# Performance work log

Measured on AMD Instinct MI355X. Metric: run time of the kernel, lower is better.

Reference implementation:

```python
import jax, jax.numpy as jnp
import numpy as np

NUM_CLASSES = 2
THRESHOLD = 0.35
NEGPOS_RATIO = 3
VAR0, VAR1 = 0.1, 0.2
ALPHA = 1.0
B, P, G = 16, 131072, 64


def _iou(a, b):
    # a: [G,4] point-form gts, b: [P,4] point-form priors -> [G,P]
    tl = jnp.maximum(a[:, None, :2], b[None, :, :2])
    br = jnp.minimum(a[:, None, 2:], b[None, :, 2:])
    wh = jnp.clip(br - tl, 0.0)
    inter = wh[..., 0] * wh[..., 1]
    area_a = (a[:, 2] - a[:, 0]) * (a[:, 3] - a[:, 1])
    area_b = (b[:, 2] - b[:, 0]) * (b[:, 3] - b[:, 1])
    return inter / (area_a[:, None] + area_b[None, :] - inter)


def setup_inputs() -> dict:
    key = jax.random.key(0)
    k1, k2, k3, k4, k5, k6 = jax.random.split(key, 6)
    loc_preds = jax.random.normal(k1, (B, P, 4), jnp.float32)
    cls_preds = jax.random.normal(k2, (B, P, NUM_CLASSES), jnp.float32)
    # priors in center form [cx, cy, w, h]
    pcxy = jax.random.uniform(k3, (P, 2), jnp.float32)
    pwh = 0.02 + 0.15 * jax.random.uniform(k4, (P, 2), jnp.float32)
    priorbox = jnp.concatenate([pcxy, pwh], axis=1)
    # ground-truth boxes; stored as [y1,x1,y2,x2,label] so that the module's
    # column permutation [1,0,3,2] yields valid point-form [x1,y1,x2,y2]
    xy1 = 0.8 * jax.random.uniform(k5, (B, G, 2), jnp.float32)
    wh = 0.02 + 0.1 * jax.random.uniform(k6, (B, G, 2), jnp.float32)
    xy2 = xy1 + wh
    boxes_perm = jnp.stack([xy1[..., 1], xy1[..., 0], xy2[..., 1], xy2[..., 0]], axis=-1)
    labels = jnp.ones((B, G, 1), jnp.float32)  # single foreground class (face)
    targets = jnp.concatenate([boxes_perm, labels], axis=-1)
    return {"loc_preds": loc_preds, "cls_preds": cls_preds,
            "priorbox": priorbox, "targets": targets}


def _loss(loc_preds, cls_preds, priorbox, targets):
    priors_c = priorbox[: loc_preds.shape[1], :]
    priors_pt = jnp.concatenate(
        [priors_c[:, :2] - priors_c[:, 2:] / 2,
         priors_c[:, :2] + priors_c[:, 2:] / 2], axis=1)
    num_g = targets.shape[1]

    def match_one(t):
        gts = t[:, :4][:, jnp.array([1, 0, 3, 2])]  # -> point form [x1,y1,x2,y2]
        labels = t[:, 4]
        ov = _iou(gts, priors_pt)                    # [G,P]
        best_prior_idx = jnp.argmax(ov, axis=1)      # [G]
        bto = jnp.max(ov, axis=0)                    # [P] best gt overlap per prior
        bti = jnp.argmax(ov, axis=0)                 # [P]
        bto = bto.at[best_prior_idx].set(2.0)        # force best prior per gt
        bti = bti.at[best_prior_idx].set(jnp.arange(num_g))
        conf = jnp.where(bto < THRESHOLD, 0.0, labels[bti])
        m = gts[bti]                                 # [P,4] matched gt boxes
        g_cxcy = ((m[:, :2] + m[:, 2:]) / 2 - priors_c[:, :2]) / (VAR0 * priors_c[:, 2:])
        g_wh = jnp.log((m[:, 2:] - m[:, :2]) / priors_c[:, 2:]) / VAR1
        return conf, jnp.concatenate([g_cxcy, g_wh], axis=1)

    cls_batch, loc_batch = jax.vmap(match_one)(targets)
    cls_batch = jax.lax.stop_gradient(cls_batch)   # targets require no grad
    loc_batch = jax.lax.stop_gradient(loc_batch)

    pos = cls_batch > 0                              # [B,P]
    npos = jnp.sum(pos)

    # smooth-L1 over positive priors, mean over selected elements (size_average)
    d = loc_preds - loc_batch
    ad = jnp.abs(d)
    sl1 = jnp.where(ad < 1.0, 0.5 * d * d, ad - 0.5)
    loss_loc = jnp.sum(sl1 * pos[..., None]) / jnp.maximum(npos * 4, 1).astype(sl1.dtype)

    # per-prior CE loss for hard-negative mining
    ignore = cls_batch < 0
    lbl = jnp.where(ignore, 0.0, cls_batch).astype(jnp.int32)
    lse = jax.nn.logsumexp(cls_preds, axis=-1)       # [B,P]
    gathered = jnp.take_along_axis(cls_preds, lbl[..., None], axis=-1)[..., 0]
    loss_c = jnp.where(pos | ignore, 0.0, lse - gathered)
    # two-stage sort: rank of each prior by descending loss
    loss_idx = jnp.argsort(-loss_c, axis=1)
    idx_rank = jnp.argsort(loss_idx, axis=1)
    num_pos_img = jnp.sum(pos, axis=1, keepdims=True)
    num_neg = jnp.minimum(NEGPOS_RATIO * num_pos_img, pos.shape[1] - 1)
    neg = idx_rank < num_neg
    mask = pos | neg
    # cross-entropy over mined samples, mean over selected (size_average)
    loss_cls = jnp.sum((lse - gathered) * mask) / jnp.maximum(jnp.sum(mask), 1).astype(lse.dtype)

    loss = (loss_cls + ALPHA * loss_loc) / npos.astype(lse.dtype)
    return loss, loss_loc, loss_cls


def reference(loc_preds, cls_preds, priorbox, targets):
    return _loss(loc_preds, cls_preds, priorbox, targets)
```

## Files before the change

### kernel.cpp

```cpp
#include <hip/hip_runtime.h>

#define BB 16
#define PP 131072
#define GG 64
#define THRESH 0.35f
#define RMAX 0.086f
#define NCELL 32
#define NCHM 64
#define CPM 2048
#define NCHL 64
#define CPL 2048
#define NCC 64
#define CPC 2048

#define OFF_BESTP   0
#define OFF_BEST64  524288
#define OFF_H1TOT   532480
#define OFF_NPOSP   794624
#define OFF_PCP     798720
#define OFF_LOCP    802816
#define OFF_CIDX    806912
#define OFF_NEGS    806976
#define OFF_RESN    807040
#define OFF_RESK    807104
#define OFF_RESC    807168
#define OFF_RESL    807232
#define OFF_PU8     807296
#define OFF_KEYS    2904448
#define OFF_CAND    11293056

__global__ __launch_bounds__(256) void k_match(
    const float* __restrict__ priorbox, const float* __restrict__ targets,
    unsigned long long* __restrict__ bestp, unsigned char* __restrict__ pu8,
    unsigned* __restrict__ h1tot, unsigned* __restrict__ cidx,
    float* __restrict__ negs)
{
    __shared__ unsigned msk[2 * NCELL * NCELL];
    __shared__ float4 gxy[GG];
    __shared__ unsigned long long sbest[GG];
    const int b = blockIdx.y, chunk = blockIdx.x, tid = threadIdx.x;

    if (tid < 64) h1tot[b * 4096 + chunk * 64 + tid] = 0u;
    if (chunk == 0 && tid == 0) { cidx[b] = 0u; negs[b] = 0.f; }
    for (int i = tid; i < 2 * NCELL * NCELL; i += 256) msk[i] = 0u;
    if (tid < GG) {
        const float* t = targets + (size_t)(b * GG + tid) * 5;
        gxy[tid] = make_float4(t[1], t[0], t[3], t[2]);
        sbest[tid] = 0ull;
    }
    __syncthreads();

    {
        const int g = tid & 63, strip = tid >> 6;
        float4 a = gxy[g];
        int cx0 = max(0, (int)((a.x - RMAX) * (float)NCELL));
        int cx1 = min(NCELL - 1, (int)ceilf((a.z + RMAX) * (float)NCELL) - 1);
        int cy0 = max(0, (int)((a.y - RMAX) * (float)NCELL));
        int cy1 = min(NCELL - 1, (int)ceilf((a.w + RMAX) * (float)NCELL) - 1);
        unsigned bit = 1u << (g & 31);
        const int word = (g >> 5);
        for (int cy = cy0 + strip; cy <= cy1; cy += 4)
            for (int cx = cx0; cx <= cx1; cx++)
                atomicOr(&msk[2 * (cy * NCELL + cx) + word], bit);
    }
    __syncthreads();

#pragma unroll
    for (int j = 0; j < 8; j++) {
        const int p = chunk * CPM + j * 256 + tid;
        float4 pr = *reinterpret_cast<const float4*>(priorbox + (size_t)p * 4);
        float hx = 0.5f * pr.z, hy = 0.5f * pr.w;
        float px1 = pr.x - hx, py1 = pr.y - hy;
        float px2 = pr.x + hx, py2 = pr.y + hy;
        float par = (px2 - px1) * (py2 - py1);
        int cx = min(NCELL - 1, max(0, (int)(pr.x * (float)NCELL)));
        int cy = min(NCELL - 1, max(0, (int)(pr.y * (float)NCELL)));
        uint2 mm = *reinterpret_cast<uint2*>(&msk[2 * (cy * NCELL + cx)]);
        unsigned long long m = ((unsigned long long)mm.y << 32) | mm.x;
        const unsigned long long notp = (unsigned long long)(~(unsigned)p);
        float bv = -1.f; int bg = 0;
        while (m) {
            const int g0 = __ffsll(m) - 1; m &= m - 1;
            const bool has1 = (m != 0ull);
            const int g1 = has1 ? (__ffsll(m) - 1) : g0;
            if (has1) m &= m - 1;
            float4 a0 = gxy[g0];
            float4 a1 = gxy[g1];
            float w0 = fmaxf(fminf(a0.z, px2) - fmaxf(a0.x, px1), 0.f);
            float h0 = fmaxf(fminf(a0.w, py2) - fmaxf(a0.y, py1), 0.f);
            float w1 = fmaxf(fminf(a1.z, px2) - fmaxf(a1.x, px1), 0.f);
            float h1 = fmaxf(fminf(a1.w, py2) - fmaxf(a1.y, py1), 0.f);
            float ar0 = (a0.z - a0.x) * (a0.w - a0.y);
            float ar1 = (a1.z - a1.x) * (a1.w - a1.y);
            float i0 = w0 * h0, i1 = w1 * h1;
            float v0 = i0 * __builtin_amdgcn_rcpf(ar0 + par - i0);
            float v1 = i1 * __builtin_amdgcn_rcpf(ar1 + par - i1);
            if (v0 > bv) { bv = v0; bg = g0; }
            if (has1 && v1 > bv) { bv = v1; bg = g1; }
            if (v0 > 0.f)
                atomicMax(&sbest[g0],
                          (((unsigned long long)__float_as_uint(v0)) << 32) | notp);
            if (has1 && v1 > 0.f)
                atomicMax(&sbest[g1],
                          (((unsigned long long)__float_as_uint(v1)) << 32) | notp);
        }
        pu8[(size_t)b * PP + p] = (unsigned char)(bg | ((bv >= THRESH) ? 0x80 : 0));
    }

    __syncthreads();
    if (tid < GG) bestp[(b * NCHM + chunk) * GG + tid] = sbest[tid];
}

__global__ void k_bred(const unsigned long long* __restrict__ bestp,
                       unsigned long long* __restrict__ best64)
{
    const int b = blockIdx.x, g = threadIdx.x;
    unsigned long long m = 0ull;
#pragma unroll 8
    for (int c = 0; c < NCHM; c++) {
        unsigned long long v = bestp[(b * NCHM + c) * GG + g];
        m = v > m ? v : m;
    }
    best64[b * GG + g] = m;
}

__global__ __launch_bounds__(256) void k_loss(
    const float* __restrict__ loc_preds, const float* __restrict__ cls_preds,
    const float* __restrict__ priorbox, const float* __restrict__ targets,
    const unsigned long long* __restrict__ best64, const unsigned char* __restrict__ pu8,
    unsigned* __restrict__ keys, unsigned* __restrict__ h1tot,
    int* __restrict__ nposp, float* __restrict__ pcp, float* __restrict__ locp)
{
    __shared__ unsigned hcnt[4096];
    __shared__ unsigned ovr[CPL];
    __shared__ float4 gxy[GG];
    __shared__ float glab[GG];
    __shared__ float sred[8];
    __shared__ int sredi[4];
    const int b = blockIdx.y, chunk = blockIdx.x, tid = threadIdx.x;
    const int lane = tid & 63, wid = tid >> 6;

    for (int i = tid; i < 4096; i += 256) hcnt[i] = 0u;
    for (int i = tid; i < CPL; i += 256) ovr[i] = 0u;
    if (tid < GG) {
        const float* t = targets + (size_t)(b * GG + tid) * 5;
        gxy[tid] = make_float4(t[1], t[0], t[3], t[2]);
        glab[tid] = t[4];
    }
    __syncthreads();
    if (tid < GG) {
        unsigned long long m = best64[b * GG + tid];
        if (m) {
            unsigned p = ~((unsigned)(m & 0xFFFFFFFFull));
            if ((int)(p >> 11) == chunk)
                atomicMax(&ovr[p & (CPL - 1)], (unsigned)tid + 1u);
        }
    }
    __syncthreads();

    float locpart = 0.f, clspart = 0.f; int cnt = 0;
#pragma unroll
    for (int j = 0; j < 8; j++) {
        const int plocal = j * 256 + tid;
        const size_t ip = (size_t)b * PP + chunk * CPL + plocal;
        const unsigned m8 = pu8[ip];
        int g = m8 & 63;
        bool pos = (m8 >> 7) != 0;
        const unsigned o = ovr[plocal];
        if (o) { pos = true; g = (int)o - 1; }
        const float2 cl = *reinterpret_cast<const float2*>(cls_preds + ip * 2);
        const float mx = fmaxf(cl.x, cl.y);
        const float lse = mx + log1pf(expf(fminf(cl.x, cl.y) - mx));
        unsigned key = 0u;
        if (pos && glab[g] > 0.f) {
            float gathered = (((int)glab[g]) == 0) ? cl.x : cl.y;
            clspart += lse - gathered;
            cnt++;
            const int p = chunk * CPL + plocal;
            float4 pr = *reinterpret_cast<const float4*>(priorbox + (size_t)p * 4);
            float4 gt = gxy[g];
            float gcx = ((gt.x + gt.z) * 0.5f - pr.x) / (0.1f * pr.z);
            float gcy = ((gt.y + gt.w) * 0.5f - pr.y) / (0.1f * pr.w);
            float gw = logf((gt.z - gt.x) / pr.z) / 0.2f;
            float gh = logf((gt.w - gt.y) / pr.w) / 0.2f;
            float4 lp = *reinterpret_cast<const float4*>(loc_preds + ip * 4);
            float d0 = lp.x - gcx, d1 = lp.y - gcy, d2 = lp.z - gw, d3 = lp.w - gh;
            float a0 = fabsf(d0), a1 = fabsf(d1), a2 = fabsf(d2), a3 = fabsf(d3);
            locpart += ((a0 < 1.f) ? 0.5f * d0 * d0 : a0 - 0.5f)
                     + ((a1 < 1.f) ? 0.5f * d1 * d1 : a1 - 0.5f)
                     + ((a2 < 1.f) ? 0.5f * d2 * d2 : a2 - 0.5f)
                     + ((a3 < 1.f) ? 0.5f * d3 * d3 : a3 - 0.5f);
        } else {
            float lc = lse - cl.x;
            key = __float_as_uint(lc);
            atomicAdd(&hcnt[key >> 20], 1u);
        }
        keys[ip] = key;
    }

    for (int o = 32; o; o >>= 1) {
        locpart += __shfl_xor(locpart, o);
        clspart += __shfl_xor(clspart, o);
        cnt     += __shfl_xor(cnt, o);
    }
    if (lane == 0) { sred[wid] = locpart; sred[4 + wid] = clspart; sredi[wid] = cnt; }
    __syncthreads();
    if (tid == 0) {
        float l = sred[0] + sred[1] + sred[2] + sred[3];
        float c = sred[4] + sred[5] + sred[6] + sred[7];
        int n = sredi[0] + sredi[1] + sredi[2] + sredi[3];
        nposp[b * NCHL + chunk] = n;
        pcp[b * NCHL + chunk] = c;
        locp[b * NCHL + chunk] = l;
    }
    __syncthreads();
    for (int i = tid; i < 4096; i += 256) {
        unsigned cc = hcnt[i];
        if (cc) atomicAdd(&h1tot[b * 4096 + i], cc);
    }
}

template <int NBINS>
__device__ void find_kth_par(const unsigned* __restrict__ h, int k, int* sel, int* krem)
{
    constexpr int PER = NBINS / 256;
    __shared__ unsigned wsum_[4];
    __shared__ int res_[2];
    const int tid = threadIdx.x, lane = tid & 63, wid = tid >> 6;
    __syncthreads();
    unsigned s = 0;
#pragma unroll
    for (int i = 0; i < PER; i++) s += h[NBINS - 1 - (tid * PER + i)];
    unsigned incl = s;
    for (int d = 1; d < 64; d <<= 1) {
        unsigned t = __shfl_up(incl, d);
        if (lane >= d) incl += t;
    }
    if (lane == 63) wsum_[wid] = incl;
    if (tid == 0) { res_[0] = -1; res_[1] = 0; }
    __syncthreads();
    unsigned woff = 0;
    for (int w = 0; w < 4; w++) woff += (w < wid) ? wsum_[w] : 0u;
    const unsigned texcl = woff + incl - s;
    if (k > 0 && texcl < (unsigned)k && texcl + s >= (unsigned)k) {
        unsigned run = texcl;
        for (int i = 0; i < PER; i++) {
            unsigned hv = h[NBINS - 1 - (tid * PER + i)];
            run += hv;
            if (run >= (unsigned)k) {
                res_[0] = NBINS - 1 - (tid * PER + i);
                res_[1] = k - (int)(run - hv);
                break;
            }
        }
    }
    __syncthreads();
    *sel = res_[0]; *krem = res_[1];
}

__device__ float block_sum_f(float v)
{
    __shared__ float rs[4];
    const int tid = threadIdx.x;
    __syncthreads();
    for (int o = 32; o; o >>= 1) v += __shfl_xor(v, o);
    if ((tid & 63) == 0) rs[tid >> 6] = v;
    __syncthreads();
    return rs[0] + rs[1] + rs[2] + rs[3];
}

__device__ int np_of_image(const int* __restrict__ nposp, int b)
{
    __shared__ int snp;
    const int tid = threadIdx.x;
    int v = (tid < 64) ? nposp[b * NCHL + tid] : 0;
    if (tid < 64) {
        for (int o = 32; o; o >>= 1) v += __shfl_xor(v, o);
        if (tid == 0) snp = v;
    }
    __syncthreads();
    return snp;
}

__global__ __launch_bounds__(256) void k_compact(
    const unsigned* __restrict__ keys, const unsigned* __restrict__ h1tot,
    const int* __restrict__ nposp, unsigned* __restrict__ cand,
    unsigned* __restrict__ cidx, float* __restrict__ negs)
{
    __shared__ unsigned wcnt[4], wbase[4];
    __shared__ unsigned bbase;
    const int b = blockIdx.y, chunk = blockIdx.x, tid = threadIdx.x;
    const int lane = tid & 63, wid = tid >> 6;

    unsigned kv[8];
#pragma unroll
    for (int j = 0; j < 8; j++)
        kv[j] = keys[(size_t)b * PP + chunk * CPC + j * 256 + tid];

    const int np = np_of_image(nposp, b);
    const int k = min(3 * np, PP - 1);
    int sel1, kk1;
    find_kth_par<4096>(h1tot + b * 4096, k, &sel1, &kk1);
    const unsigned s1 = (unsigned)sel1;

    float nv = 0.f;
    if (sel1 >= 0) {
#pragma unroll
        for (int j = 0; j < 8; j++)
            if ((kv[j] >> 20) > s1) nv += __uint_as_float(kv[j]);
    }
    float nsum = block_sum_f(nv);
    if (tid == 0 && nsum != 0.f) atomicAdd(&negs[b], nsum);

    unsigned long long mv[8];
    unsigned wn = 0;
#pragma unroll
    for (int j = 0; j < 8; j++) {
        mv[j] = __ballot((kv[j] >> 20) == s1);
        wn += (unsigned)__popcll(mv[j]);
    }
    if (lane == 0) wcnt[wid] = wn;
    __syncthreads();
    if (tid == 0) {
        unsigned run = 0;
        for (int w = 0; w < 4; w++) { wbase[w] = run; run += wcnt[w]; }
        bbase = run ? atomicAdd(&cidx[b], run) : 0u;
    }
    __syncthreads();
    unsigned run = bbase + wbase[wid];
    const unsigned long long lanemask = (1ull << lane) - 1ull;
#pragma unroll
    for (int j = 0; j < 8; j++) {
        if ((kv[j] >> 20) == s1)
            cand[(size_t)b * PP + run + (unsigned)__popcll(mv[j] & lanemask)] = kv[j];
        run += (unsigned)__popcll(mv[j]);
    }
}

__global__ __launch_bounds__(256) void k_select(
    const unsigned* __restrict__ cand, const unsigned* __restrict__ cidx,
    const unsigned* __restrict__ h1tot, const int* __restrict__ nposp,
    const float* __restrict__ pcp, const float* __restrict__ locp,
    const float* __restrict__ negs,
    int* __restrict__ resn, int* __restrict__ resk,
    float* __restrict__ resc, float* __restrict__ resl)
{
    __shared__ unsigned ch[1024];
    __shared__ float cs[1024];
    const int b = blockIdx.x, tid = threadIdx.x;

    const int np = np_of_image(nposp, b);
    const int k = min(3 * np, PP - 1);
    int sel1, kk1;
    find_kth_par<4096>(h1tot + b * 4096, k, &sel1, &kk1);
    const unsigned ncand = cidx[b];

    float pv = (tid < 64) ? pcp[b * NCHL + tid] : 0.f;
    float lv = (tid < 64) ? locp[b * NCHL + tid] : 0.f;
    float pcsum = block_sum_f(pv);
    float locsum = block_sum_f(lv);

    for (int i = tid; i < 1024; i += 256) { ch[i] = 0u; cs[i] = 0.f; }
    __syncthreads();
    for (unsigned i = tid; i < ncand; i += 256) {
        unsigned v = cand[(size_t)b * PP + i];
        unsigned bin = (v >> 10) & 1023u;
        atomicAdd(&ch[bin], 1u);
        atomicAdd(&cs[bin], __uint_as_float(v));
    }
    __syncthreads();
    int sel2, kk2;
    find_kth_par<1024>(ch, (sel1 < 0) ? 0 : kk1, &sel2, &kk2);
    float s2v = 0.f;
    for (int i = tid * 4; i < tid * 4 + 4; i++)
        if (sel2 >= 0 && i > sel2) s2v += cs[i];
    float sumhi2 = block_sum_f(s2v);

    __syncthreads();
    for (int i = tid; i < 1024; i += 256) { ch[i] = 0u; cs[i] = 0.f; }
    __syncthreads();
    if (sel2 >= 0) {
        for (unsigned i = tid; i < ncand; i += 256) {
            unsigned v = cand[(size_t)b * PP + i];
            if (((v >> 10) & 1023u) == (unsigned)sel2) {
                atomicAdd(&ch[v & 1023u], 1u);
                atomicAdd(&cs[v & 1023u], __uint_as_float(v));
            }
        }
    }
    __syncthreads();
    int sel3, needeq;
    find_kth_par<1024>(ch, (sel2 < 0) ? 0 : kk2, &sel3, &needeq);
    float s3v = 0.f;
    for (int i = tid * 4; i < tid * 4 + 4; i++)
        if (sel3 >= 0 && i > sel3) s3v += cs[i];
    float sumhi3 = block_sum_f(s3v);

    if (tid == 0) {
        float add = 0.f;
        if (sel3 >= 0 && needeq > 0) {
            unsigned Kstar = ((unsigned)sel1 << 20) | ((unsigned)sel2 << 10) | (unsigned)sel3;
            add = needeq * __uint_as_float(Kstar);
        }
        resn[b] = np;
        resk[b] = k;
        resc[b] = pcsum + negs[b] + sumhi2 + sumhi3 + add;
        resl[b] = locsum;
    }
}

__global__ void k_final(const int* __restrict__ resn, const int* __restrict__ resk,
                        const float* __restrict__ resc, const float* __restrict__ resl,
                        float* __restrict__ out)
{
    const int t = threadIdx.x;
    int n = 0, kk = 0; float c = 0.f, l = 0.f;
    if (t < BB) { n = resn[t]; kk = resk[t]; c = resc[t]; l = resl[t]; }
    for (int o = 8; o; o >>= 1) {
        n += __shfl_xor(n, o); kk += __shfl_xor(kk, o);
        c += __shfl_xor(c, o); l += __shfl_xor(l, o);
    }
    if (t == 0) {
        long long maskc = (long long)n + kk;
        float denom_loc = (float)((4 * n > 1) ? 4 * n : 1);
        float denom_cls = (float)((maskc > 1) ? maskc : 1);
        float loss_loc = l / denom_loc;
        float loss_cls = c / denom_cls;
        out[0] = (loss_cls + loss_loc) / (float)n;
        out[1] = loss_loc;
        out[2] = loss_cls;
    }
}

extern "C" void kernel_launch(void* const* d_in, const int* in_sizes, int n_in,
                              void* d_out, int out_size, void* d_ws, size_t ws_size,
                              hipStream_t stream)
{
    const float* loc_preds = (const float*)d_in[0];
    const float* cls_preds = (const float*)d_in[1];
    const float* priorbox  = (const float*)d_in[2];
    const float* targets   = (const float*)d_in[3];
    float* out = (float*)d_out;

    char* ws = (char*)d_ws;
    unsigned long long* bestp  = (unsigned long long*)(ws + OFF_BESTP);
    unsigned long long* best64 = (unsigned long long*)(ws + OFF_BEST64);
    unsigned* h1tot = (unsigned*)(ws + OFF_H1TOT);
    int*      nposp = (int*)(ws + OFF_NPOSP);
    float*    pcp   = (float*)(ws + OFF_PCP);
    float*    locp  = (float*)(ws + OFF_LOCP);
    unsigned* cidx  = (unsigned*)(ws + OFF_CIDX);
    float*    negs  = (float*)(ws + OFF_NEGS);
    int*      resn  = (int*)(ws + OFF_RESN);
    int*      resk  = (int*)(ws + OFF_RESK);
    float*    resc  = (float*)(ws + OFF_RESC);
    float*    resl  = (float*)(ws + OFF_RESL);
    unsigned char* pu8 = (unsigned char*)(ws + OFF_PU8);
    unsigned* keys  = (unsigned*)(ws + OFF_KEYS);
    unsigned* cand  = (unsigned*)(ws + OFF_CAND);

    k_match<<<dim3(NCHM, BB), 256, 0, stream>>>(priorbox, targets, bestp, pu8,
                                                h1tot, cidx, negs);
    k_bred<<<BB, 64, 0, stream>>>(bestp, best64);
    k_loss<<<dim3(NCHL, BB), 256, 0, stream>>>(loc_preds, cls_preds, priorbox, targets,
                                               best64, pu8, keys, h1tot,
                                               nposp, pcp, locp);
    k_compact<<<dim3(NCC, BB), 256, 0, stream>>>(keys, h1tot, nposp, cand, cidx, negs);
    k_select<<<BB, 256, 0, stream>>>(cand, cidx, h1tot, nposp, pcp, locp, negs,
                                     resn, resk, resc, resl);
    k_final<<<1, 64, 0, stream>>>(resn, resk, resc, resl, out);
}
```

Baseline: 100.5 us.

## Fold small reduction kernels into neighbours and split match into two passes

Removes the k_bred launch by having each k_loss block reduce the per-chunk best-prior table itself. Removes the k_final launch with a last-block-done atomic counter in k_select. Replaces the 64-bit LDS atomicMax in k_match with a 32-bit max of IoU values, followed by a second pass that recomputes IoU and takes atomicMin of the prior index for ties. This trades two launches and the wider atomics for a duplicated IoU pass and redundant 64-chunk reductions in every k_loss block.

```diff
diff --git a/kernel.cpp b/kernel.cpp
--- a/kernel.cpp
+++ b/kernel.cpp
@@ -14,39 +14,41 @@
 #define CPC 2048
 
 #define OFF_BESTP   0
-#define OFF_BEST64  524288
-#define OFF_H1TOT   532480
-#define OFF_NPOSP   794624
-#define OFF_PCP     798720
-#define OFF_LOCP    802816
-#define OFF_CIDX    806912
-#define OFF_NEGS    806976
-#define OFF_RESN    807040
-#define OFF_RESK    807104
-#define OFF_RESC    807168
-#define OFF_RESL    807232
-#define OFF_PU8     807296
-#define OFF_KEYS    2904448
-#define OFF_CAND    11293056
+#define OFF_H1TOT   524288
+#define OFF_NPOSP   786432
+#define OFF_PCP     790528
+#define OFF_LOCP    794624
+#define OFF_CIDX    798720
+#define OFF_NEGS    798784
+#define OFF_DONE    798848
+#define OFF_RESN    798912
+#define OFF_RESK    798976
+#define OFF_RESC    799040
+#define OFF_RESL    799104
+#define OFF_PU8     799168
+#define OFF_KEYS    2896320
+#define OFF_CAND    11284928
 
 __global__ __launch_bounds__(256) void k_match(
     const float* __restrict__ priorbox, const float* __restrict__ targets,
     unsigned long long* __restrict__ bestp, unsigned char* __restrict__ pu8,
     unsigned* __restrict__ h1tot, unsigned* __restrict__ cidx,
-    float* __restrict__ negs)
+    float* __restrict__ negs, unsigned* __restrict__ done)
 {
     __shared__ unsigned msk[2 * NCELL * NCELL];
     __shared__ float4 gxy[GG];
-    __shared__ unsigned long long sbest[GG];
+    __shared__ unsigned sbv[GG];
+    __shared__ unsigned sbp[GG];
     const int b = blockIdx.y, chunk = blockIdx.x, tid = threadIdx.x;
 
     if (tid < 64) h1tot[b * 4096 + chunk * 64 + tid] = 0u;
-    if (chunk == 0 && tid == 0) { cidx[b] = 0u; negs[b] = 0.f; }
+    if (chunk == 0 && tid == 0) { cidx[b] = 0u; negs[b] = 0.f; if (b == 0) *done = 0u; }
     for (int i = tid; i < 2 * NCELL * NCELL; i += 256) msk[i] = 0u;
     if (tid < GG) {
         const float* t = targets + (size_t)(b * GG + tid) * 5;
         gxy[tid] = make_float4(t[1], t[0], t[3], t[2]);
-        sbest[tid] = 0ull;
+        sbv[tid] = 0u;
+        sbp[tid] = 0xFFFFFFFFu;
     }
     __syncthreads();
 
@@ -75,59 +77,67 @@
         float par = (px2 - px1) * (py2 - py1);
         int cx = min(NCELL - 1, max(0, (int)(pr.x * (float)NCELL)));
         int cy = min(NCELL - 1, max(0, (int)(pr.y * (float)NCELL)));
-        uint2 mm = *reinterpret_cast<uint2*>(&msk[2 * (cy * NCELL + cx)]);
-        unsigned long long m = ((unsigned long long)mm.y << 32) | mm.x;
-        const unsigned long long notp = (unsigned long long)(~(unsigned)p);
+        unsigned m0 = msk[2 * (cy * NCELL + cx)];
+        unsigned m1 = msk[2 * (cy * NCELL + cx) + 1];
         float bv = -1.f; int bg = 0;
-        while (m) {
-            const int g0 = __ffsll(m) - 1; m &= m - 1;
-            const bool has1 = (m != 0ull);
-            const int g1 = has1 ? (__ffsll(m) - 1) : g0;
-            if (has1) m &= m - 1;
-            float4 a0 = gxy[g0];
-            float4 a1 = gxy[g1];
-            float w0 = fmaxf(fminf(a0.z, px2) - fmaxf(a0.x, px1), 0.f);
-            float h0 = fmaxf(fminf(a0.w, py2) - fmaxf(a0.y, py1), 0.f);
-            float w1 = fmaxf(fminf(a1.z, px2) - fmaxf(a1.x, px1), 0.f);
-            float h1 = fmaxf(fminf(a1.w, py2) - fmaxf(a1.y, py1), 0.f);
-            float ar0 = (a0.z - a0.x) * (a0.w - a0.y);
-            float ar1 = (a1.z - a1.x) * (a1.w - a1.y);
-            float i0 = w0 * h0, i1 = w1 * h1;
-            float v0 = i0 * __builtin_amdgcn_rcpf(ar0 + par - i0);
-            float v1 = i1 * __builtin_amdgcn_rcpf(ar1 + par - i1);
-            if (v0 > bv) { bv = v0; bg = g0; }
-            if (has1 && v1 > bv) { bv = v1; bg = g1; }
-            if (v0 > 0.f)
-                atomicMax(&sbest[g0],
-                          (((unsigned long long)__float_as_uint(v0)) << 32) | notp);
-            if (has1 && v1 > 0.f)
-                atomicMax(&sbest[g1],
-                          (((unsigned long long)__float_as_uint(v1)) << 32) | notp);
-        }
+#define VISIT1(GIDX)                                                        \
+        {                                                                   \
+            float4 a = gxy[GIDX];                                           \
+            float w = fmaxf(fminf(a.z, px2) - fmaxf(a.x, px1), 0.f);        \
+            float h = fmaxf(fminf(a.w, py2) - fmaxf(a.y, py1), 0.f);        \
+            float inter = w * h;                                            \
+            float ar = (a.z - a.x) * (a.w - a.y);                           \
+            float v = inter * __builtin_amdgcn_rcpf(ar + par - inter);      \
+            if (v > bv) { bv = v; bg = (GIDX); }                            \
+            if (v > 0.f) atomicMax(&sbv[GIDX], __float_as_uint(v));         \
+        }
+        while (m0) { const int g = __ffs(m0) - 1; m0 &= m0 - 1; VISIT1(g); }
+        while (m1) { const int g = 32 + __ffs(m1) - 1; m1 &= m1 - 1; VISIT1(g); }
+#undef VISIT1
         pu8[(size_t)b * PP + p] = (unsigned char)(bg | ((bv >= THRESH) ? 0x80 : 0));
     }
-
-    __syncthreads();
-    if (tid < GG) bestp[(b * NCHM + chunk) * GG + tid] = sbest[tid];
-}
-
-__global__ void k_bred(const unsigned long long* __restrict__ bestp,
-                       unsigned long long* __restrict__ best64)
-{
-    const int b = blockIdx.x, g = threadIdx.x;
-    unsigned long long m = 0ull;
-#pragma unroll 8
-    for (int c = 0; c < NCHM; c++) {
-        unsigned long long v = bestp[(b * NCHM + c) * GG + g];
-        m = v > m ? v : m;
-    }
-    best64[b * GG + g] = m;
+    __syncthreads();
+
+#pragma unroll
+    for (int j = 0; j < 8; j++) {
+        const int p = chunk * CPM + j * 256 + tid;
+        float4 pr = *reinterpret_cast<const float4*>(priorbox + (size_t)p * 4);
+        float hx = 0.5f * pr.z, hy = 0.5f * pr.w;
+        float px1 = pr.x - hx, py1 = pr.y - hy;
+        float px2 = pr.x + hx, py2 = pr.y + hy;
+        float par = (px2 - px1) * (py2 - py1);
+        int cx = min(NCELL - 1, max(0, (int)(pr.x * (float)NCELL)));
+        int cy = min(NCELL - 1, max(0, (int)(pr.y * (float)NCELL)));
+        unsigned m0 = msk[2 * (cy * NCELL + cx)];
+        unsigned m1 = msk[2 * (cy * NCELL + cx) + 1];
+#define VISIT2(GIDX)                                                        \
+        {                                                                   \
+            float4 a = gxy[GIDX];                                           \
+            float w = fmaxf(fminf(a.z, px2) - fmaxf(a.x, px1), 0.f);        \
+            float h = fmaxf(fminf(a.w, py2) - fmaxf(a.y, py1), 0.f);        \
+            float inter = w * h;                                            \
+            float ar = (a.z - a.x) * (a.w - a.y);                           \
+            float v = inter * __builtin_amdgcn_rcpf(ar + par - inter);      \
+            if (v > 0.f && __float_as_uint(v) == sbv[GIDX])                 \
+                atomicMin(&sbp[GIDX], (unsigned)p);                         \
+        }
+        while (m0) { const int g = __ffs(m0) - 1; m0 &= m0 - 1; VISIT2(g); }
+        while (m1) { const int g = 32 + __ffs(m1) - 1; m1 &= m1 - 1; VISIT2(g); }
+#undef VISIT2
+    }
+    __syncthreads();
+    if (tid < GG) {
+        unsigned v = sbv[tid];
+        bestp[(b * NCHM + chunk) * GG + tid] =
+            v ? ((((unsigned long long)v) << 32) |
+                 (unsigned long long)(~sbp[tid])) : 0ull;
+    }
 }
 
 __global__ __launch_bounds__(256) void k_loss(
     const float* __restrict__ loc_preds, const float* __restrict__ cls_preds,
     const float* __restrict__ priorbox, const float* __restrict__ targets,
-    const unsigned long long* __restrict__ best64, const unsigned char* __restrict__ pu8,
+    const unsigned long long* __restrict__ bestp, const unsigned char* __restrict__ pu8,
     unsigned* __restrict__ keys, unsigned* __restrict__ h1tot,
     int* __restrict__ nposp, float* __restrict__ pcp, float* __restrict__ locp)
 {
@@ -149,7 +159,12 @@
     }
     __syncthreads();
     if (tid < GG) {
-        unsigned long long m = best64[b * GG + tid];
+        unsigned long long m = 0ull;
+#pragma unroll 8
+        for (int c = 0; c < NCHM; c++) {
+            unsigned long long v = bestp[(b * NCHM + c) * GG + tid];
+            m = v > m ? v : m;
+        }
         if (m) {
             unsigned p = ~((unsigned)(m & 0xFFFFFFFFull));
             if ((int)(p >> 11) == chunk)
@@ -343,10 +358,12 @@
     const float* __restrict__ pcp, const float* __restrict__ locp,
     const float* __restrict__ negs,
     int* __restrict__ resn, int* __restrict__ resk,
-    float* __restrict__ resc, float* __restrict__ resl)
+    float* __restrict__ resc, float* __restrict__ resl,
+    unsigned* __restrict__ done, float* __restrict__ out)
 {
     __shared__ unsigned ch[1024];
     __shared__ float cs[1024];
+    __shared__ int lastflag;
     const int b = blockIdx.x, tid = threadIdx.x;
 
     const int np = np_of_image(nposp, b);
@@ -406,21 +423,23 @@
         resk[b] = k;
         resc[b] = pcsum + negs[b] + sumhi2 + sumhi3 + add;
         resl[b] = locsum;
-    }
-}
-
-__global__ void k_final(const int* __restrict__ resn, const int* __restrict__ resk,
-                        const float* __restrict__ resc, const float* __restrict__ resl,
-                        float* __restrict__ out)
-{
-    const int t = threadIdx.x;
+        __threadfence();
+        lastflag = (atomicAdd(done, 1u) == BB - 1) ? 1 : 0;
+    }
+    __syncthreads();
+    if (!lastflag) return;
+    if (tid == 0) __threadfence();
+    __syncthreads();
+
     int n = 0, kk = 0; float c = 0.f, l = 0.f;
-    if (t < BB) { n = resn[t]; kk = resk[t]; c = resc[t]; l = resl[t]; }
-    for (int o = 8; o; o >>= 1) {
-        n += __shfl_xor(n, o); kk += __shfl_xor(kk, o);
-        c += __shfl_xor(c, o); l += __shfl_xor(l, o);
-    }
-    if (t == 0) {
+    if (tid < BB) { n = resn[tid]; kk = resk[tid]; c = resc[tid]; l = resl[tid]; }
+    if (tid < 64) {
+        for (int o = 8; o; o >>= 1) {
+            n += __shfl_xor(n, o); kk += __shfl_xor(kk, o);
+            c += __shfl_xor(c, o); l += __shfl_xor(l, o);
+        }
+    }
+    if (tid == 0) {
         long long maskc = (long long)n + kk;
         float denom_loc = (float)((4 * n > 1) ? 4 * n : 1);
         float denom_cls = (float)((maskc > 1) ? maskc : 1);
@@ -443,14 +462,14 @@
     float* out = (float*)d_out;
 
     char* ws = (char*)d_ws;
-    unsigned long long* bestp  = (unsigned long long*)(ws + OFF_BESTP);
-    unsigned long long* best64 = (unsigned long long*)(ws + OFF_BEST64);
+    unsigned long long* bestp = (unsigned long long*)(ws + OFF_BESTP);
     unsigned* h1tot = (unsigned*)(ws + OFF_H1TOT);
     int*      nposp = (int*)(ws + OFF_NPOSP);
     float*    pcp   = (float*)(ws + OFF_PCP);
     float*    locp  = (float*)(ws + OFF_LOCP);
     unsigned* cidx  = (unsigned*)(ws + OFF_CIDX);
     float*    negs  = (float*)(ws + OFF_NEGS);
+    unsigned* done  = (unsigned*)(ws + OFF_DONE);
     int*      resn  = (int*)(ws + OFF_RESN);
     int*      resk  = (int*)(ws + OFF_RESK);
     float*    resc  = (float*)(ws + OFF_RESC);
@@ -460,13 +479,11 @@
     unsigned* cand  = (unsigned*)(ws + OFF_CAND);
 
     k_match<<<dim3(NCHM, BB), 256, 0, stream>>>(priorbox, targets, bestp, pu8,
-                                                h1tot, cidx, negs);
-    k_bred<<<BB, 64, 0, stream>>>(bestp, best64);
+                                                h1tot, cidx, negs, done);
     k_loss<<<dim3(NCHL, BB), 256, 0, stream>>>(loc_preds, cls_preds, priorbox, targets,
-                                               best64, pu8, keys, h1tot,
+                                               bestp, pu8, keys, h1tot,
                                                nposp, pcp, locp);
     k_compact<<<dim3(NCC, BB), 256, 0, stream>>>(keys, h1tot, nposp, cand, cidx, negs);
     k_select<<<BB, 256, 0, stream>>>(cand, cidx, h1tot, nposp, pcp, locp, negs,
-                                     resn, resk, resc, resl);
-    k_final<<<1, 64, 0, stream>>>(resn, resk, resc, resl, out);
-}
+                                     resn, resk, resc, resl, done, out);
+}
```

After: 125.4 us. 1.25x slower.

## Use size-dependent spatial grid masks and fold reduction/final kernels into neighbors

Applied to the files above, without the earlier changes.

Builds two per-cell GT bitmasks in k_match, one with a small expansion radius for priors whose half-extent is below a bound and one with the original large radius, so small priors test fewer GT candidates. It also folds the per-image best-prior reduction (k_bred) into k_loss, where each block redundantly reduces 64 partials, and folds k_final into k_select using a last-block atomic counter. The aim is to cut IoU work and remove two kernel launches, at the cost of doubled mask setup, redundant partial reads per k_loss block, and a fence-based last-block pattern.

```diff
diff --git a/kernel.cpp b/kernel.cpp
--- a/kernel.cpp
+++ b/kernel.cpp
@@ -4,7 +4,9 @@
 #define PP 131072
 #define GG 64
 #define THRESH 0.35f
-#define RMAX 0.086f
+#define EXPL 0.086f
+#define EXPS 0.0495f
+#define CLSB 0.049f
 #define NCELL 32
 #define NCHM 64
 #define CPM 2048
@@ -14,35 +16,36 @@
 #define CPC 2048
 
 #define OFF_BESTP   0
-#define OFF_BEST64  524288
-#define OFF_H1TOT   532480
-#define OFF_NPOSP   794624
-#define OFF_PCP     798720
-#define OFF_LOCP    802816
-#define OFF_CIDX    806912
-#define OFF_NEGS    806976
-#define OFF_RESN    807040
-#define OFF_RESK    807104
-#define OFF_RESC    807168
-#define OFF_RESL    807232
-#define OFF_PU8     807296
-#define OFF_KEYS    2904448
-#define OFF_CAND    11293056
+#define OFF_H1TOT   524288
+#define OFF_NPOSP   786432
+#define OFF_PCP     790528
+#define OFF_LOCP    794624
+#define OFF_CIDX    798720
+#define OFF_NEGS    798784
+#define OFF_DONE    798848
+#define OFF_RESN    798912
+#define OFF_RESK    798976
+#define OFF_RESC    799040
+#define OFF_RESL    799104
+#define OFF_PU8     799168
+#define OFF_KEYS    2896320
+#define OFF_CAND    11284928
 
 __global__ __launch_bounds__(256) void k_match(
     const float* __restrict__ priorbox, const float* __restrict__ targets,
     unsigned long long* __restrict__ bestp, unsigned char* __restrict__ pu8,
     unsigned* __restrict__ h1tot, unsigned* __restrict__ cidx,
-    float* __restrict__ negs)
-{
-    __shared__ unsigned msk[2 * NCELL * NCELL];
+    float* __restrict__ negs, unsigned* __restrict__ done)
+{
+    __shared__ unsigned mskS[2 * NCELL * NCELL];
+    __shared__ unsigned mskL[2 * NCELL * NCELL];
     __shared__ float4 gxy[GG];
     __shared__ unsigned long long sbest[GG];
     const int b = blockIdx.y, chunk = blockIdx.x, tid = threadIdx.x;
 
     if (tid < 64) h1tot[b * 4096 + chunk * 64 + tid] = 0u;
-    if (chunk == 0 && tid == 0) { cidx[b] = 0u; negs[b] = 0.f; }
-    for (int i = tid; i < 2 * NCELL * NCELL; i += 256) msk[i] = 0u;
+    if (chunk == 0 && tid == 0) { cidx[b] = 0u; negs[b] = 0.f; if (b == 0) *done = 0u; }
+    for (int i = tid; i < 2 * NCELL * NCELL; i += 256) { mskS[i] = 0u; mskL[i] = 0u; }
     if (tid < GG) {
         const float* t = targets + (size_t)(b * GG + tid) * 5;
         gxy[tid] = make_float4(t[1], t[0], t[3], t[2]);
@@ -53,15 +56,26 @@
     {
         const int g = tid & 63, strip = tid >> 6;
         float4 a = gxy[g];
-        int cx0 = max(0, (int)((a.x - RMAX) * (float)NCELL));
-        int cx1 = min(NCELL - 1, (int)ceilf((a.z + RMAX) * (float)NCELL) - 1);
-        int cy0 = max(0, (int)((a.y - RMAX) * (float)NCELL));
-        int cy1 = min(NCELL - 1, (int)ceilf((a.w + RMAX) * (float)NCELL) - 1);
         unsigned bit = 1u << (g & 31);
-        const int word = (g >> 5);
-        for (int cy = cy0 + strip; cy <= cy1; cy += 4)
-            for (int cx = cx0; cx <= cx1; cx++)
-                atomicOr(&msk[2 * (cy * NCELL + cx) + word], bit);
+        const int word = g >> 5;
+        {
+            int cx0 = max(0, (int)((a.x - EXPS) * (float)NCELL));
+            int cx1 = min(NCELL - 1, (int)ceilf((a.z + EXPS) * (float)NCELL) - 1);
+            int cy0 = max(0, (int)((a.y - EXPS) * (float)NCELL));
+            int cy1 = min(NCELL - 1, (int)ceilf((a.w + EXPS) * (float)NCELL) - 1);
+            for (int cy = cy0 + strip; cy <= cy1; cy += 4)
+                for (int cx = cx0; cx <= cx1; cx++)
+                    atomicOr(&mskS[2 * (cy * NCELL + cx) + word], bit);
+        }
+        {
+            int cx0 = max(0, (int)((a.x - EXPL) * (float)NCELL));
+            int cx1 = min(NCELL - 1, (int)ceilf((a.z + EXPL) * (float)NCELL) - 1);
+            int cy0 = max(0, (int)((a.y - EXPL) * (float)NCELL));
+            int cy1 = min(NCELL - 1, (int)ceilf((a.w + EXPL) * (float)NCELL) - 1);
+            for (int cy = cy0 + strip; cy <= cy1; cy += 4)
+                for (int cx = cx0; cx <= cx1; cx++)
+                    atomicOr(&mskL[2 * (cy * NCELL + cx) + word], bit);
+        }
     }
     __syncthreads();
 
@@ -75,7 +89,8 @@
         float par = (px2 - px1) * (py2 - py1);
         int cx = min(NCELL - 1, max(0, (int)(pr.x * (float)NCELL)));
         int cy = min(NCELL - 1, max(0, (int)(pr.y * (float)NCELL)));
-        uint2 mm = *reinterpret_cast<uint2*>(&msk[2 * (cy * NCELL + cx)]);
+        const unsigned* mb = (fmaxf(hx, hy) <= CLSB) ? mskS : mskL;
+        uint2 mm = *reinterpret_cast<const uint2*>(&mb[2 * (cy * NCELL + cx)]);
         unsigned long long m = ((unsigned long long)mm.y << 32) | mm.x;
         const unsigned long long notp = (unsigned long long)(~(unsigned)p);
         float bv = -1.f; int bg = 0;
@@ -111,23 +126,10 @@
     if (tid < GG) bestp[(b * NCHM + chunk) * GG + tid] = sbest[tid];
 }
 
-__global__ void k_bred(const unsigned long long* __restrict__ bestp,
-                       unsigned long long* __restrict__ best64)
-{
-    const int b = blockIdx.x, g = threadIdx.x;
-    unsigned long long m = 0ull;
-#pragma unroll 8
-    for (int c = 0; c < NCHM; c++) {
-        unsigned long long v = bestp[(b * NCHM + c) * GG + g];
-        m = v > m ? v : m;
-    }
-    best64[b * GG + g] = m;
-}
-
 __global__ __launch_bounds__(256) void k_loss(
     const float* __restrict__ loc_preds, const float* __restrict__ cls_preds,
     const float* __restrict__ priorbox, const float* __restrict__ targets,
-    const unsigned long long* __restrict__ best64, const unsigned char* __restrict__ pu8,
+    const unsigned long long* __restrict__ bestp, const unsigned char* __restrict__ pu8,
     unsigned* __restrict__ keys, unsigned* __restrict__ h1tot,
     int* __restrict__ nposp, float* __restrict__ pcp, float* __restrict__ locp)
 {
@@ -149,7 +151,12 @@
     }
     __syncthreads();
     if (tid < GG) {
-        unsigned long long m = best64[b * GG + tid];
+        unsigned long long m = 0ull;
+#pragma unroll 8
+        for (int c = 0; c < NCHM; c++) {
+            unsigned long long v = bestp[(b * NCHM + c) * GG + tid];
+            m = v > m ? v : m;
+        }
         if (m) {
             unsigned p = ~((unsigned)(m & 0xFFFFFFFFull));
             if ((int)(p >> 11) == chunk)
@@ -343,10 +350,12 @@
     const float* __restrict__ pcp, const float* __restrict__ locp,
     const float* __restrict__ negs,
     int* __restrict__ resn, int* __restrict__ resk,
-    float* __restrict__ resc, float* __restrict__ resl)
+    float* __restrict__ resc, float* __restrict__ resl,
+    unsigned* __restrict__ done, float* __restrict__ out)
 {
     __shared__ unsigned ch[1024];
     __shared__ float cs[1024];
+    __shared__ int lastflag;
     const int b = blockIdx.x, tid = threadIdx.x;
 
     const int np = np_of_image(nposp, b);
@@ -406,21 +415,23 @@
         resk[b] = k;
         resc[b] = pcsum + negs[b] + sumhi2 + sumhi3 + add;
         resl[b] = locsum;
-    }
-}
-
-__global__ void k_final(const int* __restrict__ resn, const int* __restrict__ resk,
-                        const float* __restrict__ resc, const float* __restrict__ resl,
-                        float* __restrict__ out)
-{
-    const int t = threadIdx.x;
+        __threadfence();
+        lastflag = (atomicAdd(done, 1u) == BB - 1) ? 1 : 0;
+    }
+    __syncthreads();
+    if (!lastflag) return;
+    if (tid == 0) __threadfence();
+    __syncthreads();
+
     int n = 0, kk = 0; float c = 0.f, l = 0.f;
-    if (t < BB) { n = resn[t]; kk = resk[t]; c = resc[t]; l = resl[t]; }
-    for (int o = 8; o; o >>= 1) {
-        n += __shfl_xor(n, o); kk += __shfl_xor(kk, o);
-        c += __shfl_xor(c, o); l += __shfl_xor(l, o);
-    }
-    if (t == 0) {
+    if (tid < BB) { n = resn[tid]; kk = resk[tid]; c = resc[tid]; l = resl[tid]; }
+    if (tid < 64) {
+        for (int o = 8; o; o >>= 1) {
+            n += __shfl_xor(n, o); kk += __shfl_xor(kk, o);
+            c += __shfl_xor(c, o); l += __shfl_xor(l, o);
+        }
+    }
+    if (tid == 0) {
         long long maskc = (long long)n + kk;
         float denom_loc = (float)((4 * n > 1) ? 4 * n : 1);
         float denom_cls = (float)((maskc > 1) ? maskc : 1);
@@ -443,14 +454,14 @@
     float* out = (float*)d_out;
 
     char* ws = (char*)d_ws;
-    unsigned long long* bestp  = (unsigned long long*)(ws + OFF_BESTP);
-    unsigned long long* best64 = (unsigned long long*)(ws + OFF_BEST64);
+    unsigned long long* bestp = (unsigned long long*)(ws + OFF_BESTP);
     unsigned* h1tot = (unsigned*)(ws + OFF_H1TOT);
     int*      nposp = (int*)(ws + OFF_NPOSP);
     float*    pcp   = (float*)(ws + OFF_PCP);
     float*    locp  = (float*)(ws + OFF_LOCP);
     unsigned* cidx  = (unsigned*)(ws + OFF_CIDX);
     float*    negs  = (float*)(ws + OFF_NEGS);
+    unsigned* done  = (unsigned*)(ws + OFF_DONE);
     int*      resn  = (int*)(ws + OFF_RESN);
     int*      resk  = (int*)(ws + OFF_RESK);
     float*    resc  = (float*)(ws + OFF_RESC);
@@ -460,13 +471,11 @@
     unsigned* cand  = (unsigned*)(ws + OFF_CAND);
 
     k_match<<<dim3(NCHM, BB), 256, 0, stream>>>(priorbox, targets, bestp, pu8,
-                                                h1tot, cidx, negs);
-    k_bred<<<BB, 64, 0, stream>>>(bestp, best64);
+                                                h1tot, cidx, negs, done);
     k_loss<<<dim3(NCHL, BB), 256, 0, stream>>>(loc_preds, cls_preds, priorbox, targets,
-                                               best64, pu8, keys, h1tot,
+                                               bestp, pu8, keys, h1tot,
                                                nposp, pcp, locp);
     k_compact<<<dim3(NCC, BB), 256, 0, stream>>>(keys, h1tot, nposp, cand, cidx, negs);
     k_select<<<BB, 256, 0, stream>>>(cand, cidx, h1tot, nposp, pcp, locp, negs,
-                                     resn, resk, resc, resl);
-    k_final<<<1, 64, 0, stream>>>(resn, resk, resc, resl, out);
-}
+                                     resn, resk, resc, resl, done, out);
+}
```

After: 99.50 us. No clear change (-1.0%).
